# Performance work log

Measured on AMD Instinct MI355X. Metric: run time of the kernel, lower is better.

Reference implementation:

```python
import jax, jax.numpy as jnp
import numpy as np

DIM = 256          # dim_m == dim_d (required by hist @ W1)
HIST = 200         # history_num
B = 2048
U_TOT = 100000
V_TOT = 100000
EPS = 1e-12


def _max_norm_lookup(table, idx):
    # torch nn.Embedding(max_norm=1): rows are renormalized to L2 norm <= 1 at lookup.
    g = table[idx]
    n = jnp.linalg.norm(g, axis=-1, keepdims=True)
    return g * jnp.minimum(1.0, 1.0 / jnp.maximum(n, EPS))


def _l2norm(x):
    # F.normalize(x, 2, -1)
    return x / jnp.maximum(jnp.linalg.norm(x, axis=-1, keepdims=True), EPS)


def setup_inputs() -> dict:
    key = jax.random.key(0)
    ks = jax.random.split(key, 12)
    xav = float(np.sqrt(6.0 / (DIM + DIM)))
    xav_pb = float(np.sqrt(6.0 / (HIST + DIM)))
    return {
        "batch_u": jax.random.randint(ks[0], (B,), 0, U_TOT),
        "batch_v": jax.random.randint(ks[1], (B,), 0, V_TOT),
        "batch_history": jax.random.randint(ks[2], (B, HIST), 0, V_TOT),
        "batch_olc": jax.random.randint(ks[3], (B,), 0, 68),
        "batch_cluster_olc": jax.random.randint(ks[4], (B,), 0, 68),
        "user_emb": jax.random.normal(ks[5], (U_TOT, DIM), jnp.float32),
        "venue_emb": jax.random.normal(ks[6], (V_TOT, DIM), jnp.float32),
        "W1": jax.random.uniform(ks[7], (DIM, DIM), jnp.float32, -xav, xav),
        "W2": jax.random.uniform(ks[8], (DIM, DIM), jnp.float32, -xav, xav),
        "P": jax.random.normal(ks[9], (HIST, DIM), jnp.float32),
        "bias": jax.random.uniform(ks[10], (HIST, DIM), jnp.float32, -xav_pb, xav_pb),
        "a": jax.random.normal(ks[11], (1,), jnp.float32),
    }


def reference(batch_u, batch_v, batch_history, batch_olc, batch_cluster_olc,
              user_emb, venue_emb, W1, W2, P, bias, a):
    # batch_olc / batch_cluster_olc are read but unused in the original forward.
    u = _max_norm_lookup(user_emb, batch_u)            # [B, D]
    v = _max_norm_lookup(venue_emb, batch_v)           # [B, D]
    hist = _max_norm_lookup(venue_emb, batch_history)  # [B, H, D]

    # h = tanh(hist @ W1 + (P @ W2) + bias), broadcast over batch
    h = jnp.tanh(jnp.einsum('bhd,de->bhe', hist, W1) + (P @ W2)[None] + bias[None])
    alpha = jax.nn.softmax(h, axis=1)                  # softmax over history dim
    l = jnp.sum(alpha * hist, axis=1) + a              # [B, D], scalar a broadcast

    # TransE-style score with p_norm = 2
    s = _l2norm(u) + _l2norm(l) - _l2norm(v)
    return jnp.sqrt(jnp.sum(s * s, axis=-1))           # [B]
```

## Files before the change

kernel.cpp:

```cpp
#include <hip/hip_runtime.h>
#include <hip/hip_bf16.h>

#define DIM 256
#define HIST 200
#define MROWS 208
#define BATCH 2048
#define EPSF 1e-12f

typedef __bf16 bf16x8 __attribute__((ext_vector_type(8)));
typedef float f32x4 __attribute__((ext_vector_type(4)));

__device__ __forceinline__ unsigned short f2bf(float f) {
    union { float f; unsigned u; } v; v.f = f;
    unsigned r = (v.u + 0x7fffu + ((v.u >> 16) & 1u)) >> 16;
    return (unsigned short)r;
}
__device__ __forceinline__ unsigned pkbf(float a, float b) {
    __hip_bfloat162 t = __float22bfloat162_rn(float2{a, b});
    union { __hip_bfloat162 h; unsigned u; } v; v.h = t; return v.u;
}
__device__ __forceinline__ float bf_lo(unsigned u) {
    union { unsigned u; float f; } v; v.u = u << 16; return v.f;
}
__device__ __forceinline__ float bf_hi(unsigned u) {
    union { unsigned u; float f; } v; v.u = u & 0xffff0000u; return v.f;
}

__global__ __launch_bounds__(256) void k_prep(
    const float* __restrict__ W1, const float* __restrict__ P,
    const float* __restrict__ W2, const float* __restrict__ bias,
    unsigned short* __restrict__ W1t2, float* __restrict__ Ct2) {
    const int bid = blockIdx.x, tid = threadIdx.x;
    if (bid < 16) {
#pragma unroll
        for (int it = 0; it < 16; ++it) {
            int idx = bid * 4096 + it * 256 + tid;
            int g = idx >> 11, rem = idx & 2047;
            int n = rem >> 3, j = rem & 7;
            W1t2[idx] = f2bf(W1[(g * 8 + j) * DIM + n]);
        }
    } else {
        const int h = bid - 16;
        __shared__ float Prow[DIM];
        const int e = tid;
        float acc = 0.f;
        if (h < HIST) {
            Prow[e] = P[h * DIM + e];
            __syncthreads();
            acc = bias[h * DIM + e];
#pragma unroll 8
            for (int d = 0; d < DIM; ++d) acc += Prow[d] * W2[d * DIM + e];
        }
        if (h < 224)
            Ct2[((h >> 4) * 4 + ((h >> 2) & 3)) * 1024 + e * 4 + (h & 3)] = acc;
    }
}

template<int TILES>
__device__ __forceinline__ void process_chunk(
    int chunk_base, const int* idxS, const float* __restrict__ venue_emb,
    unsigned short* histS, const float* __restrict__ Ct2,
    const unsigned short* __restrict__ W1t2,
    int wave, int lane, int quad, int l16, int n0,
    float a_val, float* Ssum, float* Lnum) {

    const int HALF = TILES;
    const int r0 = wave * 2 * TILES;
#pragma unroll
    for (int half = 0; half < 2; ++half) {
        float4 buf[HALF];
#pragma unroll
        for (int j = 0; j < HALF; ++j)
            buf[j] = *(const float4*)(venue_emb +
                     (size_t)idxS[chunk_base + r0 + half * HALF + j] * DIM + lane * 4);
#pragma unroll
        for (int j = 0; j < HALF; ++j) {
            int lr = r0 + half * HALF + j;
            int m = chunk_base + lr;
            float4 g = buf[j];
            float ss = g.x * g.x + g.y * g.y + g.z * g.z + g.w * g.w;
            ss += __shfl_xor(ss, 1);  ss += __shfl_xor(ss, 2);  ss += __shfl_xor(ss, 4);
            ss += __shfl_xor(ss, 8);  ss += __shfl_xor(ss, 16); ss += __shfl_xor(ss, 32);
            float s = (ss > 1.f) ? __builtin_amdgcn_rsqf(ss) : 1.f;
            if (m >= HIST) s = 0.f;
            uint2 pk = { pkbf(g.x * s, g.y * s), pkbf(g.z * s, g.w * s) };
            int gr = (lane >> 1) ^ (lr & 7);
            *(uint2*)&histS[lr * 256 + gr * 8 + (lane & 1) * 4] = pk;
        }
    }
    __syncthreads();

    f32x4 acc[TILES][2];
#pragma unroll
    for (int t = 0; t < TILES; ++t)
#pragma unroll
        for (int i = 0; i < 2; ++i)
            acc[t][i] = *(const f32x4*)(Ct2 + (((chunk_base >> 4) + t) * 4 + quad) * 1024 + (n0 + i) * 4);

#pragma unroll
    for (int k = 0; k < 8; ++k) {
        bf16x8 Bf0 = *(const bf16x8*)(const void*)(W1t2 + (k * 4 + quad) * 2048 + n0 * 8);
        bf16x8 Bf1 = *(const bf16x8*)(const void*)(W1t2 + (k * 4 + quad) * 2048 + (n0 + 1) * 8);
#pragma unroll
        for (int t = 0; t < TILES; ++t) {
            int gr = (k * 4 + quad) ^ (l16 & 7);
            const bf16x8 Af = *(const bf16x8*)(const void*)(&histS[(t * 16 + l16) * 256 + gr * 8]);
            acc[t][0] = __builtin_amdgcn_mfma_f32_16x16x32_bf16(Af, Bf0, acc[t][0], 0, 0, 0);
            acc[t][1] = __builtin_amdgcn_mfma_f32_16x16x32_bf16(Af, Bf1, acc[t][1], 0, 0, 0);
        }
    }

#pragma unroll
    for (int t = 0; t < TILES; ++t)
#pragma unroll
        for (int r = 0; r < 4; ++r) {
            int lm = t * 16 + quad * 4 + r;
            int m = chunk_base + lm;
            if (m < HIST) {
                int gr = (wave * 4 + (l16 >> 2)) ^ (lm & 7);
                unsigned hv = *(const unsigned*)&histS[lm * 256 + gr * 8 + (l16 & 3) * 2];
                float x0 = acc[t][0][r], x1 = acc[t][1][r];
                float th0 = 1.f - 2.f * __builtin_amdgcn_rcpf(__expf(2.f * x0) + 1.f);
                float th1 = 1.f - 2.f * __builtin_amdgcn_rcpf(__expf(2.f * x1) + 1.f);
                float e0 = __expf(th0), e1 = __expf(th1);
                Ssum[0] += e0; Lnum[0] += e0 * bf_lo(hv);
                Ssum[1] += e1; Lnum[1] += e1 * bf_hi(hv);
            }
        }
    __syncthreads();
}

__global__ __launch_bounds__(512, 2) void k_main(
    const int* __restrict__ batch_u, const int* __restrict__ batch_v,
    const int* __restrict__ batch_history,
    const float* __restrict__ user_emb, const float* __restrict__ venue_emb,
    const float* __restrict__ Ct2, const unsigned short* __restrict__ W1t2,
    const float* __restrict__ a_ptr, float* __restrict__ out) {

    __shared__ __align__(16) unsigned short histS[112 * 256];
    __shared__ int idxS[MROWS];
    __shared__ float lArr[DIM];
    __shared__ float redS[4][4];
    __shared__ float invS[3];

    const int b = blockIdx.x;
    const int tid = threadIdx.x;
    const int wave = tid >> 6;
    const int lane = tid & 63;
    const int quad = lane >> 4;
    const int l16 = lane & 15;
    const int n0 = wave * 32 + l16 * 2;

    if (tid < MROWS)
        idxS[tid] = batch_history[b * HIST + ((tid < HIST) ? tid : 0)];
    float ut = 0.f, vt = 0.f;
    if (tid < DIM) {
        ut = user_emb[(size_t)batch_u[b] * DIM + tid];
        vt = venue_emb[(size_t)batch_v[b] * DIM + tid];
    }
    __syncthreads();

    const float a_val = a_ptr[0];
    float Ssum[2] = {0.f, 0.f}, Lnum[2] = {0.f, 0.f};

    process_chunk<7>(0,   idxS, venue_emb, histS, Ct2, W1t2,
                     wave, lane, quad, l16, n0, a_val, Ssum, Lnum);
    process_chunk<6>(112, idxS, venue_emb, histS, Ct2, W1t2,
                     wave, lane, quad, l16, n0, a_val, Ssum, Lnum);

#pragma unroll
    for (int i = 0; i < 2; ++i) {
        Ssum[i] += __shfl_xor(Ssum[i], 16); Ssum[i] += __shfl_xor(Ssum[i], 32);
        Lnum[i] += __shfl_xor(Lnum[i], 16); Lnum[i] += __shfl_xor(Lnum[i], 32);
    }
    if (quad == 0)
        *(float2*)&lArr[n0] = float2{ Lnum[0] * __builtin_amdgcn_rcpf(Ssum[0]) + a_val,
                                      Lnum[1] * __builtin_amdgcn_rcpf(Ssum[1]) + a_val };
    __syncthreads();

    const float lt = (tid < DIM) ? lArr[tid] : 0.f;
    float pu = ut * ut, pv = vt * vt, pl = lt * lt;
#pragma unroll
    for (int off = 32; off > 0; off >>= 1) {
        pu += __shfl_xor(pu, off);
        pv += __shfl_xor(pv, off);
        pl += __shfl_xor(pl, off);
    }
    if (lane == 0 && wave < 4) { redS[wave][0] = pu; redS[wave][1] = pv; redS[wave][2] = pl; }
    __syncthreads();
    if (tid == 0) {
        float su = 0.f, sv = 0.f, sl = 0.f;
        for (int w = 0; w < 4; ++w) { su += redS[w][0]; sv += redS[w][1]; sl += redS[w][2]; }
        invS[0] = 1.f / fmaxf(sqrtf(su), EPSF);
        invS[1] = 1.f / fmaxf(sqrtf(sv), EPSF);
        invS[2] = 1.f / fmaxf(sqrtf(sl), EPSF);
    }
    __syncthreads();
    float s = ut * invS[0] + lt * invS[2] - vt * invS[1];
    float s2 = s * s;
#pragma unroll
    for (int off = 32; off > 0; off >>= 1) s2 += __shfl_xor(s2, off);
    if (lane == 0 && wave < 4) redS[wave][3] = s2;
    __syncthreads();
    if (tid == 0) out[b] = sqrtf(redS[0][3] + redS[1][3] + redS[2][3] + redS[3][3]);
}

extern "C" void kernel_launch(void* const* d_in, const int* in_sizes, int n_in,
                              void* d_out, int out_size, void* d_ws, size_t ws_size,
                              hipStream_t stream) {
    const int* batch_u = (const int*)d_in[0];
    const int* batch_v = (const int*)d_in[1];
    const int* batch_history = (const int*)d_in[2];
    const float* user_emb = (const float*)d_in[5];
    const float* venue_emb = (const float*)d_in[6];
    const float* W1 = (const float*)d_in[7];
    const float* W2 = (const float*)d_in[8];
    const float* P = (const float*)d_in[9];
    const float* bias = (const float*)d_in[10];
    const float* a = (const float*)d_in[11];
    float* out = (float*)d_out;

    float* Ct2 = (float*)d_ws;
    unsigned short* W1t2 = (unsigned short*)((char*)d_ws + 229376);

    k_prep<<<240, 256, 0, stream>>>(W1, P, W2, bias, W1t2, Ct2);
    k_main<<<BATCH, 512, 0, stream>>>(batch_u, batch_v, batch_history,
                                      user_emb, venue_emb, Ct2, W1t2, a, out);
}
```

Baseline: 420.5 us.

## Precompute venue row norm scales in prep kernel and pipeline history gathers

Adds a pass in the prep kernel that computes the max-norm scale for every venue row (100k rows) into workspace. The main kernel then looks up the scale per history index instead of doing a wave-wide shuffle reduction for each gathered row. The gather loop becomes a 4-deep rolling prefetch, the k-loop is only partially unrolled, and launch bounds request 4 blocks per CU to cut register pressure. The trade-off is an extra full read of the 100 MB venue table every call, and the occupancy hint may cause spills.

New measurement: 398.7 us. -5.2%, faster.

```diff
diff --git a/kernel.cpp b/kernel.cpp
--- a/kernel.cpp
+++ b/kernel.cpp
@@ -29,7 +29,9 @@
 __global__ __launch_bounds__(256) void k_prep(
     const float* __restrict__ W1, const float* __restrict__ P,
     const float* __restrict__ W2, const float* __restrict__ bias,
-    unsigned short* __restrict__ W1t2, float* __restrict__ Ct2) {
+    const float* __restrict__ venue,
+    unsigned short* __restrict__ W1t2, float* __restrict__ Ct2,
+    float* __restrict__ sInv, int nV) {
     const int bid = blockIdx.x, tid = threadIdx.x;
     if (bid < 16) {
 #pragma unroll
@@ -39,7 +41,7 @@
             int n = rem >> 3, j = rem & 7;
             W1t2[idx] = f2bf(W1[(g * 8 + j) * DIM + n]);
         }
-    } else {
+    } else if (bid < 240) {
         const int h = bid - 16;
         __shared__ float Prow[DIM];
         const int e = tid;
@@ -51,42 +53,48 @@
 #pragma unroll 8
             for (int d = 0; d < DIM; ++d) acc += Prow[d] * W2[d * DIM + e];
         }
-        if (h < 224)
-            Ct2[((h >> 4) * 4 + ((h >> 2) & 3)) * 1024 + e * 4 + (h & 3)] = acc;
+        Ct2[((h >> 4) * 4 + ((h >> 2) & 3)) * 1024 + e * 4 + (h & 3)] = acc;
+    } else {
+        const int lane = tid & 63;
+        const int nblk = gridDim.x - 240;
+        for (int row = (bid - 240) * 4 + (tid >> 6); row < nV; row += nblk * 4) {
+            const float4 g = *(const float4*)(venue + (size_t)row * DIM + lane * 4);
+            float ss = g.x * g.x + g.y * g.y + g.z * g.z + g.w * g.w;
+#pragma unroll
+            for (int off = 32; off > 0; off >>= 1) ss += __shfl_xor(ss, off);
+            if (lane == 0) sInv[row] = (ss > 1.f) ? __builtin_amdgcn_rsqf(ss) : 1.f;
+        }
     }
 }
 
 template<int TILES>
 __device__ __forceinline__ void process_chunk(
-    int chunk_base, const int* idxS, const float* __restrict__ venue_emb,
+    int chunk_base, const int* idxS, const float* scaleS,
+    const float* __restrict__ venue_emb,
     unsigned short* histS, const float* __restrict__ Ct2,
     const unsigned short* __restrict__ W1t2,
     int wave, int lane, int quad, int l16, int n0,
-    float a_val, float* Ssum, float* Lnum) {
-
-    const int HALF = TILES;
-    const int r0 = wave * 2 * TILES;
-#pragma unroll
-    for (int half = 0; half < 2; ++half) {
-        float4 buf[HALF];
-#pragma unroll
-        for (int j = 0; j < HALF; ++j)
-            buf[j] = *(const float4*)(venue_emb +
-                     (size_t)idxS[chunk_base + r0 + half * HALF + j] * DIM + lane * 4);
-#pragma unroll
-        for (int j = 0; j < HALF; ++j) {
-            int lr = r0 + half * HALF + j;
-            int m = chunk_base + lr;
-            float4 g = buf[j];
-            float ss = g.x * g.x + g.y * g.y + g.z * g.z + g.w * g.w;
-            ss += __shfl_xor(ss, 1);  ss += __shfl_xor(ss, 2);  ss += __shfl_xor(ss, 4);
-            ss += __shfl_xor(ss, 8);  ss += __shfl_xor(ss, 16); ss += __shfl_xor(ss, 32);
-            float s = (ss > 1.f) ? __builtin_amdgcn_rsqf(ss) : 1.f;
-            if (m >= HIST) s = 0.f;
-            uint2 pk = { pkbf(g.x * s, g.y * s), pkbf(g.z * s, g.w * s) };
-            int gr = (lane >> 1) ^ (lr & 7);
-            *(uint2*)&histS[lr * 256 + gr * 8 + (lane & 1) * 4] = pk;
-        }
+    float* Ssum, float* Lnum) {
+
+    const int ROWS = TILES * 2;
+    const int r0 = wave * ROWS;
+
+    float4 buf[4];
+#pragma unroll
+    for (int j = 0; j < 4; ++j)
+        buf[j] = *(const float4*)(venue_emb +
+                 (size_t)idxS[chunk_base + r0 + j] * DIM + lane * 4);
+#pragma unroll
+    for (int j = 0; j < ROWS; ++j) {
+        float4 g = buf[j & 3];
+        if (j + 4 < ROWS)
+            buf[j & 3] = *(const float4*)(venue_emb +
+                         (size_t)idxS[chunk_base + r0 + j + 4] * DIM + lane * 4);
+        int lr = r0 + j;
+        float s = scaleS[chunk_base + lr];
+        uint2 pk = { pkbf(g.x * s, g.y * s), pkbf(g.z * s, g.w * s) };
+        int gr = (lane >> 1) ^ (lr & 7);
+        *(uint2*)&histS[lr * 256 + gr * 8 + (lane & 1) * 4] = pk;
     }
     __syncthreads();
 
@@ -97,13 +105,13 @@
         for (int i = 0; i < 2; ++i)
             acc[t][i] = *(const f32x4*)(Ct2 + (((chunk_base >> 4) + t) * 4 + quad) * 1024 + (n0 + i) * 4);
 
-#pragma unroll
+#pragma unroll 2
     for (int k = 0; k < 8; ++k) {
         bf16x8 Bf0 = *(const bf16x8*)(const void*)(W1t2 + (k * 4 + quad) * 2048 + n0 * 8);
         bf16x8 Bf1 = *(const bf16x8*)(const void*)(W1t2 + (k * 4 + quad) * 2048 + (n0 + 1) * 8);
+        int gr = (k * 4 + quad) ^ (l16 & 7);
 #pragma unroll
         for (int t = 0; t < TILES; ++t) {
-            int gr = (k * 4 + quad) ^ (l16 & 7);
             const bf16x8 Af = *(const bf16x8*)(const void*)(&histS[(t * 16 + l16) * 256 + gr * 8]);
             acc[t][0] = __builtin_amdgcn_mfma_f32_16x16x32_bf16(Af, Bf0, acc[t][0], 0, 0, 0);
             acc[t][1] = __builtin_amdgcn_mfma_f32_16x16x32_bf16(Af, Bf1, acc[t][1], 0, 0, 0);
@@ -130,15 +138,17 @@
     __syncthreads();
 }
 
-__global__ __launch_bounds__(512, 2) void k_main(
+__global__ __launch_bounds__(512, 4) void k_main(
     const int* __restrict__ batch_u, const int* __restrict__ batch_v,
     const int* __restrict__ batch_history,
     const float* __restrict__ user_emb, const float* __restrict__ venue_emb,
     const float* __restrict__ Ct2, const unsigned short* __restrict__ W1t2,
+    const float* __restrict__ sInv,
     const float* __restrict__ a_ptr, float* __restrict__ out) {
 
     __shared__ __align__(16) unsigned short histS[112 * 256];
     __shared__ int idxS[MROWS];
+    __shared__ float scaleS[MROWS];
     __shared__ float lArr[DIM];
     __shared__ float redS[4][4];
     __shared__ float invS[3];
@@ -151,8 +161,11 @@
     const int l16 = lane & 15;
     const int n0 = wave * 32 + l16 * 2;
 
-    if (tid < MROWS)
-        idxS[tid] = batch_history[b * HIST + ((tid < HIST) ? tid : 0)];
+    if (tid < MROWS) {
+        int ix = batch_history[b * HIST + ((tid < HIST) ? tid : 0)];
+        idxS[tid] = ix;
+        scaleS[tid] = (tid < HIST) ? sInv[ix] : 0.f;
+    }
     float ut = 0.f, vt = 0.f;
     if (tid < DIM) {
         ut = user_emb[(size_t)batch_u[b] * DIM + tid];
@@ -160,14 +173,14 @@
     }
     __syncthreads();
 
+    float Ssum[2] = {0.f, 0.f}, Lnum[2] = {0.f, 0.f};
+
+    process_chunk<7>(0,   idxS, scaleS, venue_emb, histS, Ct2, W1t2,
+                     wave, lane, quad, l16, n0, Ssum, Lnum);
+    process_chunk<6>(112, idxS, scaleS, venue_emb, histS, Ct2, W1t2,
+                     wave, lane, quad, l16, n0, Ssum, Lnum);
+
     const float a_val = a_ptr[0];
-    float Ssum[2] = {0.f, 0.f}, Lnum[2] = {0.f, 0.f};
-
-    process_chunk<7>(0,   idxS, venue_emb, histS, Ct2, W1t2,
-                     wave, lane, quad, l16, n0, a_val, Ssum, Lnum);
-    process_chunk<6>(112, idxS, venue_emb, histS, Ct2, W1t2,
-                     wave, lane, quad, l16, n0, a_val, Ssum, Lnum);
-
 #pragma unroll
     for (int i = 0; i < 2; ++i) {
         Ssum[i] += __shfl_xor(Ssum[i], 16); Ssum[i] += __shfl_xor(Ssum[i], 32);
@@ -220,10 +233,13 @@
     const float* a = (const float*)d_in[11];
     float* out = (float*)d_out;
 
+    const int nV = in_sizes[6] / DIM;
+
     float* Ct2 = (float*)d_ws;
     unsigned short* W1t2 = (unsigned short*)((char*)d_ws + 229376);
-
-    k_prep<<<240, 256, 0, stream>>>(W1, P, W2, bias, W1t2, Ct2);
+    float* sInv = (float*)((char*)d_ws + 229376 + 131072);
+
+    k_prep<<<752, 256, 0, stream>>>(W1, P, W2, bias, venue_emb, W1t2, Ct2, sInv, nV);
     k_main<<<BATCH, 512, 0, stream>>>(batch_u, batch_v, batch_history,
-                                      user_emb, venue_emb, Ct2, W1t2, a, out);
-}
+                                      user_emb, venue_emb, Ct2, W1t2, sInv, a, out);
+}
```
